# Kernel tuning notes

Hardware: AMD Instinct MI355X
Metric: run time of the kernel (lower is better)

Reference implementation:

```python
import jax, jax.numpy as jnp
import numpy as np


def setup_inputs() -> dict:
    key = jax.random.key(0)
    k1, k2, k3, k4, k5 = jax.random.split(key, 5)
    B, S, E, U = 32, 2048, 1024, 1024
    last_hidden_state = jax.random.normal(k1, (B, S, E), dtype=jnp.float32)
    attention_mask = jax.random.randint(k2, (B, S), 0, 2, dtype=jnp.int32)
    # ensure at least one valid token per row to avoid all -inf softmax
    attention_mask = attention_mask.at[:, 0].set(1)
    W = jax.random.normal(k3, (U, E), dtype=jnp.float32) * (E ** -0.5)
    Umat = jax.random.normal(k4, (U, E), dtype=jnp.float32) * (E ** -0.5)
    v = jax.random.normal(k5, (1, U), dtype=jnp.float32) * (U ** -0.5)
    return {"last_hidden_state": last_hidden_state, "attention_mask": attention_mask,
            "W": W, "U": Umat, "v": v}


def reference(last_hidden_state, attention_mask, W, U, v):
    # last_hidden_state: [B,S,E]; W,U: [units,E]; v: [1,units]
    Q = jnp.einsum('bse,ue->bsu', last_hidden_state, W)
    K = jnp.einsum('bse,ue->bsu', last_hidden_state, U)
    H = jnp.tanh(Q + K)                                   # [B,S,units]
    E = jnp.einsum('bsu,ou->bso', H, v)                   # [B,S,1]
    neg_inf = jnp.array(-jnp.inf, dtype=E.dtype)
    E = jnp.where(attention_mask[:, :, None] == 0, neg_inf, E)
    alpha = jax.nn.softmax(E, axis=1)                     # softmax over seq dim
    return jnp.sum(alpha * last_hidden_state, axis=1)     # [B,E]
```

## Files before the change

### kernel.cpp

```cpp
#include <hip/hip_runtime.h>
#include <hip/hip_bf16.h>


typedef short bf16x8 __attribute__((ext_vector_type(8)));
typedef float f32x4  __attribute__((ext_vector_type(4)));
typedef unsigned short u16x8 __attribute__((ext_vector_type(8)));

static __device__ __forceinline__ unsigned short f2bf(float f) {
    unsigned int x = __float_as_uint(f);
    unsigned int r = x + 0x7FFFu + ((x >> 16) & 1u);
    return (unsigned short)(r >> 16);
}

static __device__ __forceinline__ float fast_tanh(float x) {
    float e = __builtin_amdgcn_exp2f(x * 2.885390082f);
    float r = __builtin_amdgcn_rcpf(e + 1.0f);
    return __builtin_fmaf(-2.0f, r, 1.0f);
}

__global__ __launch_bounds__(256)
void prep_kernel(const float* __restrict__ W, const float* __restrict__ U,
                 unsigned short* __restrict__ wsum,
                 float* __restrict__ score, float* __restrict__ alpha,
                 float* __restrict__ out) {
    int g = blockIdx.x * 256 + threadIdx.x;
    int i4 = g * 4;
    float4 w = *(const float4*)&W[i4];
    float4 u = *(const float4*)&U[i4];
    ushort4 h;
    h.x = f2bf(w.x + u.x); h.y = f2bf(w.y + u.y);
    h.z = f2bf(w.z + u.z); h.w = f2bf(w.w + u.w);
    *(ushort4*)&wsum[i4] = h;
    if (g < 65536) { score[g] = 0.0f; alpha[g] = 0.0f; }
    if (g < 32768) out[g] = 0.0f;
}

__global__ __launch_bounds__(256)
void index_kernel(const int* __restrict__ mask, unsigned short* __restrict__ ridx,
                  int* __restrict__ cnt) {
    int b = blockIdx.x, t = threadIdx.x;
    const int* mrow = mask + b * 2048;
    int m[8], c = 0;
#pragma unroll
    for (int j = 0; j < 8; ++j) { m[j] = mrow[t * 8 + j]; c += (m[j] != 0); }
    __shared__ int sc[256];
    sc[t] = c;
    __syncthreads();
    for (int off = 1; off < 256; off <<= 1) {
        int v = (t >= off) ? sc[t - off] : 0;
        __syncthreads();
        sc[t] += v;
        __syncthreads();
    }
    int base = sc[t] - c;
    unsigned short* rb = ridx + b * 2048;
#pragma unroll
    for (int j = 0; j < 8; ++j)
        if (m[j]) rb[base++] = (unsigned short)(t * 8 + j);
    if (t == 255) cnt[b] = sc[255];
}

__global__ __launch_bounds__(256)
void gather_convert(const float* __restrict__ lhs, const unsigned short* __restrict__ ridx,
                    const int* __restrict__ cnt, unsigned short* __restrict__ Ab) {
    int b = blockIdx.y;
    int c = cnt[b];
    int cpad = (c + 127) & ~127;
    int r = blockIdx.x * 4 + (threadIdx.x >> 6);
    int lt = threadIdx.x & 63;
    if (r >= cpad) return;
    unsigned short* dst = Ab + ((size_t)b * 2048 + r) * 1024 + lt * 16;
    if (r < c) {
        int s = ridx[b * 2048 + r];
        const float* src = lhs + ((size_t)b * 2048 + s) * 1024 + lt * 16;
        float4 a0 = *(const float4*)(src + 0);
        float4 a1 = *(const float4*)(src + 4);
        float4 a2 = *(const float4*)(src + 8);
        float4 a3 = *(const float4*)(src + 12);
        u16x8 h0, h1;
        h0[0] = f2bf(a0.x); h0[1] = f2bf(a0.y); h0[2] = f2bf(a0.z); h0[3] = f2bf(a0.w);
        h0[4] = f2bf(a1.x); h0[5] = f2bf(a1.y); h0[6] = f2bf(a1.z); h0[7] = f2bf(a1.w);
        h1[0] = f2bf(a2.x); h1[1] = f2bf(a2.y); h1[2] = f2bf(a2.z); h1[3] = f2bf(a2.w);
        h1[4] = f2bf(a3.x); h1[5] = f2bf(a3.y); h1[6] = f2bf(a3.z); h1[7] = f2bf(a3.w);
        *(u16x8*)(dst + 0) = h0;
        *(u16x8*)(dst + 8) = h1;
    } else {
        u16x8 z = (u16x8){0,0,0,0,0,0,0,0};
        *(u16x8*)(dst + 0) = z;
        *(u16x8*)(dst + 8) = z;
    }
}

__global__ __launch_bounds__(256)
void score_gemm_bf16(const unsigned short* __restrict__ Ab,
                     const unsigned short* __restrict__ Bw,
                     const float* __restrict__ v, const int* __restrict__ cnt,
                     float* __restrict__ score) {
    const int K = 1024;
    __shared__ __align__(16) unsigned short As[128 * 32];
    __shared__ __align__(16) unsigned short Bs[128 * 32];

    const int tile = (int)blockIdx.y;
    const int b    = tile >> 4;
    const int lm0  = (tile & 15) << 7;
    const int c    = cnt[b];
    if (lm0 >= ((c + 127) & ~127)) return;
    const int m0   = (b << 11) + lm0;
    const int n0   = (int)blockIdx.x * 128;

    const int t    = threadIdx.x;
    const int lane = t & 63;
    const int wave = t >> 6;
    const int wm   = (wave & 1) * 64;
    const int wn   = (wave >> 1) * 64;
    const int ml   = lane & 15;
    const int q    = lane >> 4;

    f32x4 acc[4][4];
#pragma unroll
    for (int i = 0; i < 4; ++i)
#pragma unroll
        for (int j = 0; j < 4; ++j)
            acc[i][j] = (f32x4){0.f, 0.f, 0.f, 0.f};

    const int c0 = wave * 64 + lane;
    const int c1 = (4 + wave) * 64 + lane;
    const unsigned short* ga0 = Ab + (size_t)(m0 + (c0 >> 2)) * K + (c0 & 3) * 8;
    const unsigned short* ga1 = Ab + (size_t)(m0 + (c1 >> 2)) * K + (c1 & 3) * 8;
    const unsigned short* gb0 = Bw + (size_t)(n0 + (c0 >> 2)) * K + (c0 & 3) * 8;
    const unsigned short* gb1 = Bw + (size_t)(n0 + (c1 >> 2)) * K + (c1 & 3) * 8;
    unsigned short* la0 = &As[wave * 512];
    unsigned short* la1 = &As[(4 + wave) * 512];
    unsigned short* lb0 = &Bs[wave * 512];
    unsigned short* lb1 = &Bs[(4 + wave) * 512];

    for (int kk = 0; kk < K; kk += 32) {
        __builtin_amdgcn_global_load_lds((const __attribute__((address_space(1))) unsigned int*)ga0,
                                         (__attribute__((address_space(3))) unsigned int*)la0, 16, 0, 0);
        __builtin_amdgcn_global_load_lds((const __attribute__((address_space(1))) unsigned int*)ga1,
                                         (__attribute__((address_space(3))) unsigned int*)la1, 16, 0, 0);
        __builtin_amdgcn_global_load_lds((const __attribute__((address_space(1))) unsigned int*)gb0,
                                         (__attribute__((address_space(3))) unsigned int*)lb0, 16, 0, 0);
        __builtin_amdgcn_global_load_lds((const __attribute__((address_space(1))) unsigned int*)gb1,
                                         (__attribute__((address_space(3))) unsigned int*)lb1, 16, 0, 0);
        ga0 += 32; ga1 += 32; gb0 += 32; gb1 += 32;
        __syncthreads();

        bf16x8 af[4], bf[4];
#pragma unroll
        for (int i = 0; i < 4; ++i)
            af[i] = *(const bf16x8*)&As[(wm + i * 16 + ml) * 32 + q * 8];
#pragma unroll
        for (int j = 0; j < 4; ++j)
            bf[j] = *(const bf16x8*)&Bs[(wn + j * 16 + ml) * 32 + q * 8];
#pragma unroll
        for (int i = 0; i < 4; ++i)
#pragma unroll
            for (int j = 0; j < 4; ++j)
                acc[i][j] = __builtin_amdgcn_mfma_f32_16x16x32_bf16(af[i], bf[j], acc[i][j], 0, 0, 0);
        __syncthreads();
    }

    float vw[4];
#pragma unroll
    for (int j = 0; j < 4; ++j)
        vw[j] = v[n0 + wn + j * 16 + ml];

#pragma unroll
    for (int i = 0; i < 4; ++i) {
#pragma unroll
        for (int r = 0; r < 4; ++r) {
            float val = 0.f;
#pragma unroll
            for (int j = 0; j < 4; ++j)
                val += fast_tanh(acc[i][j][r]) * vw[j];
#pragma unroll
            for (int off = 8; off > 0; off >>= 1)
                val += __shfl_xor(val, off, 64);
            if (ml == 0)
                atomicAdd(&score[m0 + wm + i * 16 + q * 4 + r], val);
        }
    }
}

#define LDSS 40
__global__ __launch_bounds__(256)
void score_gemm_f32stage(const float* __restrict__ A, const unsigned short* __restrict__ Bw,
                         const float* __restrict__ v, float* __restrict__ score) {
    const int K = 1024;
    __shared__ __align__(16) unsigned short As[128][LDSS];
    __shared__ __align__(16) unsigned short Bs[128][LDSS];
    const int n0 = (int)blockIdx.x * 128;
    const int m0 = (int)blockIdx.y * 128;
    const int t = threadIdx.x, lane = t & 63, wave = t >> 6;
    const int wm = (wave & 1) * 64, wn = (wave >> 1) * 64;
    const int ml = lane & 15, q = lane >> 4;
    f32x4 acc[4][4];
#pragma unroll
    for (int i = 0; i < 4; ++i)
#pragma unroll
        for (int j = 0; j < 4; ++j) acc[i][j] = (f32x4){0.f,0.f,0.f,0.f};
    const int sr = t >> 3, sc = (t & 7) * 4;
    for (int kk = 0; kk < K; kk += 32) {
#pragma unroll
        for (int p = 0; p < 4; ++p) {
            int r = sr + p * 32;
            float4 va = *(const float4*)&A[(size_t)(m0 + r) * K + kk + sc];
            ushort4 h; h.x = f2bf(va.x); h.y = f2bf(va.y); h.z = f2bf(va.z); h.w = f2bf(va.w);
            *(ushort4*)&As[r][sc] = h;
            ushort4 vb = *(const ushort4*)&Bw[(size_t)(n0 + r) * K + kk + sc];
            *(ushort4*)&Bs[r][sc] = vb;
        }
        __syncthreads();
        bf16x8 af[4], bf[4];
#pragma unroll
        for (int i = 0; i < 4; ++i) af[i] = *(const bf16x8*)&As[wm + i * 16 + ml][q * 8];
#pragma unroll
        for (int j = 0; j < 4; ++j) bf[j] = *(const bf16x8*)&Bs[wn + j * 16 + ml][q * 8];
#pragma unroll
        for (int i = 0; i < 4; ++i)
#pragma unroll
            for (int j = 0; j < 4; ++j)
                acc[i][j] = __builtin_amdgcn_mfma_f32_16x16x32_bf16(af[i], bf[j], acc[i][j], 0, 0, 0);
        __syncthreads();
    }
    float vw[4];
#pragma unroll
    for (int j = 0; j < 4; ++j) vw[j] = v[n0 + wn + j * 16 + ml];
#pragma unroll
    for (int i = 0; i < 4; ++i)
#pragma unroll
        for (int r = 0; r < 4; ++r) {
            float val = 0.f;
#pragma unroll
            for (int j = 0; j < 4; ++j) val += fast_tanh(acc[i][j][r]) * vw[j];
#pragma unroll
            for (int off = 8; off > 0; off >>= 1) val += __shfl_xor(val, off, 64);
            if (ml == 0) atomicAdd(&score[m0 + wm + i * 16 + q * 4 + r], val);
        }
}

__global__ __launch_bounds__(256)
void softmax_compact(const float* __restrict__ score, const unsigned short* __restrict__ ridx,
                     const int* __restrict__ cnt, float* __restrict__ alpha) {
    int b = blockIdx.x, t = threadIdx.x;
    int c = cnt[b];
    __shared__ float red[8];
    float sc[8];
    float mx = -1e30f;
#pragma unroll
    for (int i = 0; i < 8; ++i) {
        int k = i * 256 + t;
        sc[i] = (k < c) ? score[b * 2048 + k] : -1e30f;
        mx = fmaxf(mx, sc[i]);
    }
#pragma unroll
    for (int off = 32; off > 0; off >>= 1)
        mx = fmaxf(mx, __shfl_xor(mx, off, 64));
    if ((t & 63) == 0) red[t >> 6] = mx;
    __syncthreads();
    mx = fmaxf(fmaxf(red[0], red[1]), fmaxf(red[2], red[3]));
    float e[8], sum = 0.f;
#pragma unroll
    for (int i = 0; i < 8; ++i) {
        int k = i * 256 + t;
        e[i] = (k < c) ? __expf(sc[i] - mx) : 0.f;
        sum += e[i];
    }
#pragma unroll
    for (int off = 32; off > 0; off >>= 1)
        sum += __shfl_xor(sum, off, 64);
    if ((t & 63) == 0) red[4 + (t >> 6)] = sum;
    __syncthreads();
    float inv = 1.0f / (red[4] + red[5] + red[6] + red[7]);
#pragma unroll
    for (int i = 0; i < 8; ++i) {
        int k = i * 256 + t;
        if (k < c) {
            int s = ridx[b * 2048 + k];
            alpha[b * 2048 + s] = e[i] * inv;
        }
    }
}

__global__ __launch_bounds__(256)
void softmax_kernel(const float* __restrict__ score, const int* __restrict__ mask,
                    float* __restrict__ alpha) {
    const int S = 2048;
    int b = blockIdx.x, t = threadIdx.x;
    __shared__ float red[8];
    float sc[8]; int vd[8];
    float mx = -1e30f;
#pragma unroll
    for (int i = 0; i < 8; ++i) {
        int s = i * 256 + t;
        vd[i] = mask[b * S + s];
        sc[i] = score[b * S + s];
        if (vd[i]) mx = fmaxf(mx, sc[i]);
    }
#pragma unroll
    for (int off = 32; off > 0; off >>= 1)
        mx = fmaxf(mx, __shfl_xor(mx, off, 64));
    if ((t & 63) == 0) red[t >> 6] = mx;
    __syncthreads();
    mx = fmaxf(fmaxf(red[0], red[1]), fmaxf(red[2], red[3]));
    float e[8]; float sum = 0.f;
#pragma unroll
    for (int i = 0; i < 8; ++i) {
        e[i] = vd[i] ? __expf(sc[i] - mx) : 0.f;
        sum += e[i];
    }
#pragma unroll
    for (int off = 32; off > 0; off >>= 1)
        sum += __shfl_xor(sum, off, 64);
    if ((t & 63) == 0) red[4 + (t >> 6)] = sum;
    __syncthreads();
    float inv = 1.0f / (red[4] + red[5] + red[6] + red[7]);
#pragma unroll
    for (int i = 0; i < 8; ++i)
        alpha[b * S + i * 256 + t] = e[i] * inv;
}

__global__ __launch_bounds__(256)
void wsum_kernel(const float* __restrict__ lhs, const float* __restrict__ alpha,
                 float* __restrict__ out) {
    const int S = 2048, E = 1024;
    int b = blockIdx.x >> 6;
    int seg = blockIdx.x & 63;
    int t = threadIdx.x;
    int s0 = seg * 32;
    const float* base = lhs + ((size_t)b * S + s0) * E + t * 4;
    const float* ap = alpha + b * S + s0;
    float4 acc = {0.f, 0.f, 0.f, 0.f};
#pragma unroll 4
    for (int s = 0; s < 32; ++s) {
        float a = ap[s];
        if (a != 0.f) {
            float4 x = *(const float4*)(base + (size_t)s * E);
            acc.x += a * x.x; acc.y += a * x.y; acc.z += a * x.z; acc.w += a * x.w;
        }
    }
    float* o = out + b * E + t * 4;
    atomicAdd(o + 0, acc.x);
    atomicAdd(o + 1, acc.y);
    atomicAdd(o + 2, acc.z);
    atomicAdd(o + 3, acc.w);
}

extern "C" void kernel_launch(void* const* d_in, const int* in_sizes, int n_in,
                              void* d_out, int out_size, void* d_ws, size_t ws_size,
                              hipStream_t stream) {
    const float* lhs  = (const float*)d_in[0];
    const int*   mask = (const int*)d_in[1];
    const float* W    = (const float*)d_in[2];
    const float* Um   = (const float*)d_in[3];
    const float* v    = (const float*)d_in[4];
    float* out = (float*)d_out;

    char* ws = (char*)d_ws;
    unsigned short* wsum  = (unsigned short*)ws;
    float* score          = (float*)(ws + 2048u * 1024u);
    float* alpha          = (float*)(ws + 2304u * 1024u);
    unsigned short* ridx  = (unsigned short*)(ws + 2560u * 1024u);
    int* cnt              = (int*)(ws + 2688u * 1024u);
    unsigned short* Ab    = (unsigned short*)(ws + 2816u * 1024u);
    const size_t need = 2816ull * 1024ull + 65536ull * 1024ull * 2ull;

    prep_kernel<<<1024, 256, 0, stream>>>(W, Um, wsum, score, alpha, out);
    if (ws_size >= need) {
        index_kernel<<<32, 256, 0, stream>>>(mask, ridx, cnt);
        dim3 gg(512, 32);
        gather_convert<<<gg, 256, 0, stream>>>(lhs, ridx, cnt, Ab);
        dim3 g1(8, 512);
        score_gemm_bf16<<<g1, 256, 0, stream>>>(Ab, wsum, v, cnt, score);
        softmax_compact<<<32, 256, 0, stream>>>(score, ridx, cnt, alpha);
    } else {
        dim3 g1(8, 512);
        score_gemm_f32stage<<<g1, 256, 0, stream>>>(lhs, wsum, v, score);
        softmax_kernel<<<32, 256, 0, stream>>>(score, mask, alpha);
    }
    wsum_kernel<<<2048, 256, 0, stream>>>(lhs, alpha, out);
}
```

Baseline: 515.4 us.

## Use K=64 XOR-swizzled LDS tiles, grouped block order, and two-pass weighted sum

The score GEMM now stages 64-wide K slices per iteration, which halves the number of barriers. LDS chunks are XOR-swizzled to avoid bank conflicts on fragment reads. Blocks are launched on a 1D grid grouped so that 8 M-tiles share N-tiles, which is meant to improve L2 reuse. The final weighted sum is split into a partial-sum kernel and a reduction kernel that write to workspace instead of using the previous accumulation path. This raises the workspace requirement, and if the new requirement is not met the code falls back to the f32 path.

```diff
diff --git a/kernel.cpp b/kernel.cpp
--- a/kernel.cpp
+++ b/kernel.cpp
@@ -97,16 +97,19 @@
                      const float* __restrict__ v, const int* __restrict__ cnt,
                      float* __restrict__ score) {
     const int K = 1024;
-    __shared__ __align__(16) unsigned short As[128 * 32];
-    __shared__ __align__(16) unsigned short Bs[128 * 32];
-
-    const int tile = (int)blockIdx.y;
-    const int b    = tile >> 4;
-    const int lm0  = (tile & 15) << 7;
-    const int c    = cnt[b];
+    __shared__ __align__(16) unsigned short As[128 * 64];
+    __shared__ __align__(16) unsigned short Bs[128 * 64];
+
+    const int bid    = (int)blockIdx.x;
+    const int group  = bid >> 6;
+    const int mt     = (group << 3) + (bid & 7);
+    const int nI     = (bid >> 3) & 7;
+    const int b      = mt >> 4;
+    const int lm0    = (mt & 15) << 7;
+    const int c      = cnt[b];
     if (lm0 >= ((c + 127) & ~127)) return;
-    const int m0   = (b << 11) + lm0;
-    const int n0   = (int)blockIdx.x * 128;
+    const int m0     = (b << 11) + lm0;
+    const int n0     = nI << 7;
 
     const int t    = threadIdx.x;
     const int lane = t & 63;
@@ -115,6 +118,7 @@
     const int wn   = (wave >> 1) * 64;
     const int ml   = lane & 15;
     const int q    = lane >> 4;
+    const int xorv = ml & 7;
 
     f32x4 acc[4][4];
 #pragma unroll
@@ -123,41 +127,48 @@
         for (int j = 0; j < 4; ++j)
             acc[i][j] = (f32x4){0.f, 0.f, 0.f, 0.f};
 
-    const int c0 = wave * 64 + lane;
-    const int c1 = (4 + wave) * 64 + lane;
-    const unsigned short* ga0 = Ab + (size_t)(m0 + (c0 >> 2)) * K + (c0 & 3) * 8;
-    const unsigned short* ga1 = Ab + (size_t)(m0 + (c1 >> 2)) * K + (c1 & 3) * 8;
-    const unsigned short* gb0 = Bw + (size_t)(n0 + (c0 >> 2)) * K + (c0 & 3) * 8;
-    const unsigned short* gb1 = Bw + (size_t)(n0 + (c1 >> 2)) * K + (c1 & 3) * 8;
-    unsigned short* la0 = &As[wave * 512];
-    unsigned short* la1 = &As[(4 + wave) * 512];
-    unsigned short* lb0 = &Bs[wave * 512];
-    unsigned short* lb1 = &Bs[(4 + wave) * 512];
-
-    for (int kk = 0; kk < K; kk += 32) {
-        __builtin_amdgcn_global_load_lds((const __attribute__((address_space(1))) unsigned int*)ga0,
-                                         (__attribute__((address_space(3))) unsigned int*)la0, 16, 0, 0);
-        __builtin_amdgcn_global_load_lds((const __attribute__((address_space(1))) unsigned int*)ga1,
-                                         (__attribute__((address_space(3))) unsigned int*)la1, 16, 0, 0);
-        __builtin_amdgcn_global_load_lds((const __attribute__((address_space(1))) unsigned int*)gb0,
-                                         (__attribute__((address_space(3))) unsigned int*)lb0, 16, 0, 0);
-        __builtin_amdgcn_global_load_lds((const __attribute__((address_space(1))) unsigned int*)gb1,
-                                         (__attribute__((address_space(3))) unsigned int*)lb1, 16, 0, 0);
-        ga0 += 32; ga1 += 32; gb0 += 32; gb1 += 32;
-        __syncthreads();
-
-        bf16x8 af[4], bf[4];
-#pragma unroll
-        for (int i = 0; i < 4; ++i)
-            af[i] = *(const bf16x8*)&As[(wm + i * 16 + ml) * 32 + q * 8];
-#pragma unroll
-        for (int j = 0; j < 4; ++j)
-            bf[j] = *(const bf16x8*)&Bs[(wn + j * 16 + ml) * 32 + q * 8];
-#pragma unroll
-        for (int i = 0; i < 4; ++i)
+    const unsigned short* gA[4];
+    const unsigned short* gB[4];
+    unsigned short* lA[4];
+    unsigned short* lB[4];
+#pragma unroll
+    for (int p = 0; p < 4; ++p) {
+        int l   = p * 256 + wave * 64 + lane;
+        int row = l >> 3;
+        int kc  = (l & 7) ^ (row & 7);
+        gA[p] = Ab + (size_t)(m0 + row) * K + kc * 8;
+        gB[p] = Bw + (size_t)(n0 + row) * K + kc * 8;
+        lA[p] = &As[(p * 4 + wave) * 512];
+        lB[p] = &Bs[(p * 4 + wave) * 512];
+    }
+
+    for (int kk = 0; kk < K; kk += 64) {
+#pragma unroll
+        for (int p = 0; p < 4; ++p) {
+            __builtin_amdgcn_global_load_lds((const __attribute__((address_space(1))) unsigned int*)gA[p],
+                                             (__attribute__((address_space(3))) unsigned int*)lA[p], 16, 0, 0);
+            __builtin_amdgcn_global_load_lds((const __attribute__((address_space(1))) unsigned int*)gB[p],
+                                             (__attribute__((address_space(3))) unsigned int*)lB[p], 16, 0, 0);
+            gA[p] += 64; gB[p] += 64;
+        }
+        __syncthreads();
+
+#pragma unroll
+        for (int s = 0; s < 2; ++s) {
+            const int koff = ((s * 4 + q) ^ xorv) * 8;
+            bf16x8 af[4], bf[4];
+#pragma unroll
+            for (int i = 0; i < 4; ++i)
+                af[i] = *(const bf16x8*)&As[(wm + i * 16 + ml) * 64 + koff];
 #pragma unroll
             for (int j = 0; j < 4; ++j)
-                acc[i][j] = __builtin_amdgcn_mfma_f32_16x16x32_bf16(af[i], bf[j], acc[i][j], 0, 0, 0);
+                bf[j] = *(const bf16x8*)&Bs[(wn + j * 16 + ml) * 64 + koff];
+#pragma unroll
+            for (int i = 0; i < 4; ++i)
+#pragma unroll
+                for (int j = 0; j < 4; ++j)
+                    acc[i][j] = __builtin_amdgcn_mfma_f32_16x16x32_bf16(af[i], bf[j], acc[i][j], 0, 0, 0);
+        }
         __syncthreads();
     }
 
@@ -319,6 +330,40 @@
 #pragma unroll
     for (int i = 0; i < 8; ++i)
         alpha[b * S + i * 256 + t] = e[i] * inv;
+}
+
+__global__ __launch_bounds__(256)
+void wsum_partial(const float* __restrict__ lhs, const float* __restrict__ alpha,
+                  float* __restrict__ part) {
+    const int S = 2048, E = 1024;
+    int b = blockIdx.x >> 6;
+    int seg = blockIdx.x & 63;
+    int t = threadIdx.x;
+    int s0 = seg * 32;
+    const float* base = lhs + ((size_t)b * S + s0) * E + t * 4;
+    const float* ap = alpha + b * S + s0;
+    float4 acc = {0.f, 0.f, 0.f, 0.f};
+#pragma unroll 4
+    for (int s = 0; s < 32; ++s) {
+        float a = ap[s];
+        if (a != 0.f) {
+            float4 x = *(const float4*)(base + (size_t)s * E);
+            acc.x += a * x.x; acc.y += a * x.y; acc.z += a * x.z; acc.w += a * x.w;
+        }
+    }
+    *(float4*)(part + (size_t)blockIdx.x * E + t * 4) = acc;
+}
+
+__global__ __launch_bounds__(256)
+void wsum_reduce(const float* __restrict__ part, float* __restrict__ out) {
+    int b = blockIdx.x >> 2;
+    int e = (blockIdx.x & 3) * 256 + threadIdx.x;
+    const float* p = part + (size_t)b * 64 * 1024 + e;
+    float sum = 0.f;
+#pragma unroll
+    for (int s = 0; s < 64; ++s)
+        sum += p[(size_t)s * 1024];
+    out[b * 1024 + e] = sum;
 }
 
 __global__ __launch_bounds__(256)
@@ -364,20 +409,22 @@
     unsigned short* ridx  = (unsigned short*)(ws + 2560u * 1024u);
     int* cnt              = (int*)(ws + 2688u * 1024u);
     unsigned short* Ab    = (unsigned short*)(ws + 2816u * 1024u);
-    const size_t need = 2816ull * 1024ull + 65536ull * 1024ull * 2ull;
+    float* part           = (float*)(ws + 2816u * 1024u + 131072u * 1024u);
+    const size_t need = 2816ull * 1024ull + 131072ull * 1024ull + 8192ull * 1024ull;
 
     prep_kernel<<<1024, 256, 0, stream>>>(W, Um, wsum, score, alpha, out);
     if (ws_size >= need) {
         index_kernel<<<32, 256, 0, stream>>>(mask, ridx, cnt);
         dim3 gg(512, 32);
         gather_convert<<<gg, 256, 0, stream>>>(lhs, ridx, cnt, Ab);
-        dim3 g1(8, 512);
-        score_gemm_bf16<<<g1, 256, 0, stream>>>(Ab, wsum, v, cnt, score);
+        score_gemm_bf16<<<4096, 256, 0, stream>>>(Ab, wsum, v, cnt, score);
         softmax_compact<<<32, 256, 0, stream>>>(score, ridx, cnt, alpha);
+        wsum_partial<<<2048, 256, 0, stream>>>(lhs, alpha, part);
+        wsum_reduce<<<128, 256, 0, stream>>>(part, out);
     } else {
         dim3 g1(8, 512);
         score_gemm_f32stage<<<g1, 256, 0, stream>>>(lhs, wsum, v, score);
         softmax_kernel<<<32, 256, 0, stream>>>(score, mask, alpha);
-    }
-    wsum_kernel<<<2048, 256, 0, stream>>>(lhs, alpha, out);
-}
+        wsum_kernel<<<2048, 256, 0, stream>>>(lhs, alpha, out);
+    }
+}
```

Measured after the change: 521.6 us. Within noise of the previous version (+1.2%).
